# Optimization experiments

Hardware: AMD Instinct MI355X
Metric: run time of the kernel (lower is better)

The kernel has to match this reference:

```python
import jax, jax.numpy as jnp
import numpy as np

N_NODES = 100000
N_EDGES = 1600000
C_IN, C_HID, C_OUT = 32, 32, 8
N_AGENTS = 1000


def _glorot(key, shape):
    fan_in, fan_out = shape[0], shape[1]
    lim = float(np.sqrt(6.0 / (fan_in + fan_out)))
    return jax.random.uniform(key, shape, jnp.float32, -lim, lim)


def setup_inputs() -> dict:
    key = jax.random.key(0)
    ks = jax.random.split(key, 16)
    x = jax.random.normal(ks[0], (N_NODES, C_IN), jnp.float32)
    edge_index = jax.random.randint(ks[1], (2, N_EDGES), 0, N_NODES, jnp.int64)
    d = {"x": x, "edge_index": edge_index}
    dims = [(C_IN, C_HID), (C_HID, C_HID), (C_HID, C_HID)]
    for i, (di, do) in enumerate(dims, start=1):
        d[f"W_l{i}"] = _glorot(ks[2 * i], (di, do))        # neighbor (aggregated) weight
        d[f"b_l{i}"] = jnp.zeros((do,), jnp.float32)
        d[f"W_r{i}"] = _glorot(ks[2 * i + 1], (di, do))    # root/self weight (no bias)
    d["W_out"] = _glorot(ks[10], (C_HID, C_OUT))
    d["b_out"] = jnp.zeros((C_OUT,), jnp.float32)
    return d


def _sage_conv(x, src, dst, W_l, b_l, W_r):
    # mean-aggregate neighbor features at destination nodes
    msg = x[src]                                               # [E, d] gather
    summed = jax.ops.segment_sum(msg, dst, num_segments=N_NODES)
    cnt = jax.ops.segment_sum(jnp.ones((src.shape[0],), x.dtype), dst,
                              num_segments=N_NODES)
    agg = summed / jnp.maximum(cnt, 1.0)[:, None]              # deg==0 -> 0
    return agg @ W_l + b_l + x @ W_r


def reference(x, edge_index, W_l1, b_l1, W_r1, W_l2, b_l2, W_r2,
              W_l3, b_l3, W_r3, W_out, b_out):
    src, dst = edge_index[0], edge_index[1]
    h = jax.nn.relu(_sage_conv(x, src, dst, W_l1, b_l1, W_r1))
    h = jax.nn.relu(_sage_conv(h, src, dst, W_l2, b_l2, W_r2))
    h = jax.nn.relu(_sage_conv(h, src, dst, W_l3, b_l3, W_r3))
    out = h @ W_out + b_out
    return out[:N_AGENTS]
```

## Files before the change

### kernel.cpp

```cpp
#include <hip/hip_runtime.h>
#include <hip/hip_bf16.h>

#define N_NODES 100000
#define N_EDGES 1600000
#define N_AGENTS 1000

#define NB 782
#define ABLK 512
#define CHUNK (N_EDGES / ABLK)
#define CONV_BLOCKS 3125
#define FLAGS_I4 25024
#define FLAG_BLOCKS 98
#define AGRID 280

typedef short s16x8 __attribute__((ext_vector_type(8)));
typedef float f32x4 __attribute__((ext_vector_type(4)));

__device__ __forceinline__ unsigned short f2bf(float f) {
    unsigned u = __float_as_uint(f);
    u += 0x7fffu + ((u >> 16) & 1u);
    return (unsigned short)(u >> 16);
}
__device__ __forceinline__ float bflo(unsigned u) { return __uint_as_float(u << 16); }
__device__ __forceinline__ float bfhi(unsigned u) { return __uint_as_float(u & 0xffff0000u); }

__global__ __launch_bounds__(256) void hist_prep_kernel(
    const int* __restrict__ dst, int* __restrict__ partialT,
    const float* __restrict__ x, unsigned short* __restrict__ xb,
    const float* __restrict__ Wl1, const float* __restrict__ Wr1,
    const float* __restrict__ Wl2, const float* __restrict__ Wr2,
    const float* __restrict__ Wl3, const float* __restrict__ Wr3,
    unsigned short* __restrict__ Wcat, int* __restrict__ flags)
{
    int b = blockIdx.x;
    if (b < ABLK) {
        __shared__ int hist[NB];
        for (int i = threadIdx.x; i < NB; i += 256) hist[i] = 0;
        __syncthreads();
        int beg = b * CHUNK;
        for (int e = beg + threadIdx.x; e < beg + CHUNK; e += 256)
            atomicAdd(&hist[dst[e] >> 7], 1);
        __syncthreads();
        for (int i = threadIdx.x; i < NB; i += 256) partialT[i * ABLK + b] = hist[i];
    } else if (b < ABLK + CONV_BLOCKS) {
        int i = (b - ABLK) * 256 + threadIdx.x;
        float4 v = ((const float4*)x)[i];
        ((ushort4*)xb)[i] = make_ushort4(f2bf(v.x), f2bf(v.y), f2bf(v.z), f2bf(v.w));
    } else if (b < ABLK + CONV_BLOCKS + 24) {
        int gid = (b - ABLK - CONV_BLOCKS) * 256 + threadIdx.x;
        int L = gid >> 11, idx = gid & 2047;
        int k = idx >> 5, n = idx & 31;
        const float* Wl = (L == 0) ? Wl1 : (L == 1) ? Wl2 : Wl3;
        const float* Wr = (L == 0) ? Wr1 : (L == 1) ? Wr2 : Wr3;
        float v = (k < 32) ? Wl[k * 32 + n] : Wr[(k - 32) * 32 + n];
        Wcat[gid] = f2bf(v);
    } else {
        int gid = (b - ABLK - CONV_BLOCKS - 24) * 256 + threadIdx.x;
        if (gid < FLAGS_I4) ((int4*)flags)[gid] = make_int4(0, 0, 0, 0);
    }
}

__global__ __launch_bounds__(256) void bucket_prefix_kernel(
    const int* __restrict__ partialT, int* __restrict__ baseT, int* __restrict__ tot)
{
    int wave = threadIdx.x >> 6, lane = threadIdx.x & 63;
    int t = blockIdx.x * 4 + wave;
    if (t >= NB) return;
    const int4* p = (const int4*)(partialT + (size_t)t * ABLK);
    int4 u0 = p[lane * 2], u1 = p[lane * 2 + 1];
    int v0 = u0.x, v1 = u0.y, v2 = u0.z, v3 = u0.w;
    int v4 = u1.x, v5 = u1.y, v6 = u1.z, v7 = u1.w;
    int p0 = 0, p1 = v0, p2 = p1 + v1, p3 = p2 + v2;
    int p4 = p3 + v3, p5 = p4 + v4, p6 = p5 + v5, p7 = p6 + v6;
    int s = p7 + v7;
    int x = s;
    #pragma unroll
    for (int off = 1; off < 64; off <<= 1) {
        int y = __shfl_up(x, off);
        if (lane >= off) x += y;
    }
    int excl = x - s;
    int4* q = (int4*)(baseT + (size_t)t * ABLK);
    q[lane * 2]     = make_int4(excl + p0, excl + p1, excl + p2, excl + p3);
    q[lane * 2 + 1] = make_int4(excl + p4, excl + p5, excl + p6, excl + p7);
    if (lane == 63) tot[t] = x;
}

__global__ __launch_bounds__(1024) void total_scan_kernel(
    const int* __restrict__ tot, int* __restrict__ bstart)
{
    __shared__ int tmp[1024];
    int t = threadIdx.x;
    int v = (t < NB) ? tot[t] : 0;
    tmp[t] = v;
    __syncthreads();
    for (int off = 1; off < 1024; off <<= 1) {
        int u = (t >= off) ? tmp[t - off] : 0;
        __syncthreads();
        tmp[t] += u;
        __syncthreads();
    }
    if (t < NB) {
        bstart[t] = tmp[t] - v;
        if (t == NB - 1) bstart[NB] = tmp[t];
    }
}

__global__ __launch_bounds__(256) void bucket_scatter_kernel(
    const int* __restrict__ src, const int* __restrict__ dst,
    const int* __restrict__ baseT, const int* __restrict__ bstart,
    int* __restrict__ ebuf)
{
    __shared__ int cur[NB];
    int b = blockIdx.x;
    for (int i = threadIdx.x; i < NB; i += 256)
        cur[i] = bstart[i] + baseT[(size_t)i * ABLK + b];
    __syncthreads();
    int beg = b * CHUNK;
    for (int e = beg + threadIdx.x; e < beg + CHUNK; e += 256) {
        int d = dst[e];
        int slot = atomicAdd(&cur[d >> 7], 1);
        ebuf[slot] = src[e] | ((d & 127) << 17);
    }
}

__global__ __launch_bounds__(256) void bucket_csr_kernel(
    const int* __restrict__ bstart, const int* __restrict__ ebuf,
    int* __restrict__ rowptr, float* __restrict__ inv, int* __restrict__ esrc)
{
    __shared__ int hist4[512], cur4[512], tmp[256];
    int b = blockIdx.x;
    int t = threadIdx.x;
    int beg = bstart[b], end = bstart[b + 1];
    hist4[t] = 0; hist4[t + 256] = 0;
    __syncthreads();
    for (int i = beg + t; i < end; i += 256) {
        int p = ebuf[i];
        int ln = (p >> 17) & 127;
        int cls = (p & 0x1FFFF) >> 15;
        atomicAdd(&hist4[ln * 4 + cls], 1);
    }
    __syncthreads();
    int c0 = 0, c1 = 0, c2 = 0, c3 = 0, v = 0;
    if (t < 128) {
        c0 = hist4[t * 4 + 0]; c1 = hist4[t * 4 + 1];
        c2 = hist4[t * 4 + 2]; c3 = hist4[t * 4 + 3];
        v = c0 + c1 + c2 + c3;
    }
    tmp[t] = v;
    __syncthreads();
    for (int off = 1; off < 256; off <<= 1) {
        int u = (t >= off) ? tmp[t - off] : 0;
        __syncthreads();
        tmp[t] += u;
        __syncthreads();
    }
    int excl = tmp[t] - v;
    int node = b * 128 + t;
    if (t < 128 && node < N_NODES) {
        int start = beg + excl;
        rowptr[node] = start;
        inv[node] = 1.0f / fmaxf((float)v, 1.0f);
        cur4[t * 4 + 0] = start;
        cur4[t * 4 + 1] = start + c0;
        cur4[t * 4 + 2] = start + c0 + c1;
        cur4[t * 4 + 3] = start + c0 + c1 + c2;
    }
    if (b == NB - 1 && t == 0) rowptr[N_NODES] = N_EDGES;
    __syncthreads();
    for (int i = beg + t; i < end; i += 256) {
        int p = ebuf[i];
        int ln = (p >> 17) & 127;
        int s = p & 0x1FFFF;
        int slot = atomicAdd(&cur4[ln * 4 + (s >> 15)], 1);
        esrc[slot] = s;
    }
}

__global__ __launch_bounds__(256) void active_mark_kernel(
    const int* __restrict__ rowptr, const int* __restrict__ esrc,
    int* __restrict__ flags, int* __restrict__ acount)
{
    int gid = blockIdx.x * 256 + threadIdx.x;
    if (gid == 0) *acount = 0;
    if (gid < N_AGENTS) flags[gid] = 1;
    int e1 = rowptr[N_AGENTS];
    for (int j = gid; j < e1; j += gridDim.x * 256)
        flags[esrc[j]] = 1;
}

__global__ __launch_bounds__(256) void active_compact_kernel(
    const int* __restrict__ flags, int* __restrict__ alist, int* __restrict__ acount)
{
    int gid = blockIdx.x * 256 + threadIdx.x;
    int f = (gid < N_NODES) ? flags[gid] : 0;
    int lane = threadIdx.x & 63, wave = threadIdx.x >> 6;
    unsigned long long m = __ballot(f != 0);
    int pre = __popcll(m & ((1ull << lane) - 1ull));
    __shared__ int wbase[4];
    __shared__ int bbase;
    if (lane == 0) wbase[wave] = __popcll(m);
    __syncthreads();
    if (threadIdx.x == 0) {
        int t0 = wbase[0], t1 = t0 + wbase[1], t2 = t1 + wbase[2];
        int tot = t2 + wbase[3];
        bbase = atomicAdd(acount, tot);
        wbase[0] = 0; wbase[1] = t0; wbase[2] = t1; wbase[3] = t2;
    }
    __syncthreads();
    if (f) alist[bbase + wbase[wave] + pre] = gid;
}

__global__ __launch_bounds__(256) void sage_fused_kernel(
    const int* __restrict__ rowptr, const int* __restrict__ esrc,
    const float* __restrict__ inv, const unsigned short* __restrict__ hb,
    const unsigned short* __restrict__ Wcat, const float* __restrict__ bl,
    const float* __restrict__ Wout, const float* __restrict__ bout,
    void* __restrict__ outp, int n_nodes, int final)
{
    __shared__ unsigned short sW[2048];
    __shared__ float sb[32];
    __shared__ unsigned short smean[64 * 40];
    __shared__ float sh3[64 * 33];
    __shared__ float sWo[256];
    __shared__ float sbo[8];

    int tid = threadIdx.x;
    ((uint4*)sW)[tid] = ((const uint4*)Wcat)[tid];
    if (tid < 32) sb[tid] = bl[tid];
    if (final) {
        sWo[tid] = Wout[tid];
        if (tid < 8) sbo[tid] = bout[tid];
    }

    int lane = tid & 63, wave = tid >> 6;

    int g = lane >> 2, q = lane & 3;
    int nodeA = blockIdx.x * 64 + wave * 16 + g;
    int beg = 0, end = 0;
    if (nodeA < n_nodes) { beg = rowptr[nodeA]; end = rowptr[nodeA + 1]; }
    float a0 = 0.f, a1 = 0.f, a2 = 0.f, a3 = 0.f;
    float a4 = 0.f, a5 = 0.f, a6 = 0.f, a7 = 0.f;
    int j = beg;
    for (; j + 3 < end; j += 4) {
        int s0 = esrc[j];
        int s1 = esrc[j + 1];
        int s2 = esrc[j + 2];
        int s3 = esrc[j + 3];
        uint4 u0 = *(const uint4*)(hb + s0 * 32 + q * 8);
        uint4 u1 = *(const uint4*)(hb + s1 * 32 + q * 8);
        uint4 u2 = *(const uint4*)(hb + s2 * 32 + q * 8);
        uint4 u3 = *(const uint4*)(hb + s3 * 32 + q * 8);
        a0 += bflo(u0.x); a1 += bfhi(u0.x);
        a2 += bflo(u0.y); a3 += bfhi(u0.y);
        a4 += bflo(u0.z); a5 += bfhi(u0.z);
        a6 += bflo(u0.w); a7 += bfhi(u0.w);
        a0 += bflo(u1.x); a1 += bfhi(u1.x);
        a2 += bflo(u1.y); a3 += bfhi(u1.y);
        a4 += bflo(u1.z); a5 += bfhi(u1.z);
        a6 += bflo(u1.w); a7 += bfhi(u1.w);
        a0 += bflo(u2.x); a1 += bfhi(u2.x);
        a2 += bflo(u2.y); a3 += bfhi(u2.y);
        a4 += bflo(u2.z); a5 += bfhi(u2.z);
        a6 += bflo(u2.w); a7 += bfhi(u2.w);
        a0 += bflo(u3.x); a1 += bfhi(u3.x);
        a2 += bflo(u3.y); a3 += bfhi(u3.y);
        a4 += bflo(u3.z); a5 += bfhi(u3.z);
        a6 += bflo(u3.w); a7 += bfhi(u3.w);
    }
    for (; j < end; j++) {
        int s = esrc[j];
        uint4 u = *(const uint4*)(hb + s * 32 + q * 8);
        a0 += bflo(u.x); a1 += bfhi(u.x);
        a2 += bflo(u.y); a3 += bfhi(u.y);
        a4 += bflo(u.z); a5 += bfhi(u.z);
        a6 += bflo(u.w); a7 += bfhi(u.w);
    }
    float iv = (nodeA < n_nodes) ? inv[nodeA] : 0.f;
    uint4 o;
    o.x = (unsigned)f2bf(a0 * iv) | ((unsigned)f2bf(a1 * iv) << 16);
    o.y = (unsigned)f2bf(a2 * iv) | ((unsigned)f2bf(a3 * iv) << 16);
    o.z = (unsigned)f2bf(a4 * iv) | ((unsigned)f2bf(a5 * iv) << 16);
    o.w = (unsigned)f2bf(a6 * iv) | ((unsigned)f2bf(a7 * iv) << 16);
    int mrow = wave * 16 + g;
    *(uint4*)&smean[mrow * 40 + q * 8] = o;
    __syncthreads();

    int l15 = lane & 15, quad = lane >> 4;
    s16x8 bf_[2][2];
    #pragma unroll
    for (int kt = 0; kt < 2; kt++)
        #pragma unroll
        for (int nt = 0; nt < 2; nt++)
            #pragma unroll
            for (int jj = 0; jj < 8; jj++) {
                int k = kt * 32 + quad * 8 + jj;
                bf_[kt][nt][jj] = (short)sW[k * 32 + l15 + nt * 16];
            }
    float bias0 = sb[l15], bias1 = sb[l15 + 16];

    int tilebase = blockIdx.x * 64 + wave * 16;
    int nodeD = tilebase + l15;
    int na = min(nodeD, n_nodes - 1);
    s16x8 am = *(const s16x8*)&smean[(wave * 16 + l15) * 40 + quad * 8];
    s16x8 as = *(const s16x8*)(hb + (size_t)na * 32 + quad * 8);
    f32x4 acc0 = {0.f, 0.f, 0.f, 0.f};
    f32x4 acc1 = {0.f, 0.f, 0.f, 0.f};
    acc0 = __builtin_amdgcn_mfma_f32_16x16x32_bf16(am, bf_[0][0], acc0, 0, 0, 0);
    acc0 = __builtin_amdgcn_mfma_f32_16x16x32_bf16(as, bf_[1][0], acc0, 0, 0, 0);
    acc1 = __builtin_amdgcn_mfma_f32_16x16x32_bf16(am, bf_[0][1], acc1, 0, 0, 0);
    acc1 = __builtin_amdgcn_mfma_f32_16x16x32_bf16(as, bf_[1][1], acc1, 0, 0, 0);

    if (!final) {
        #pragma unroll
        for (int r = 0; r < 4; r++) {
            int onode = tilebase + quad * 4 + r;
            if (onode < n_nodes) {
                ((unsigned short*)outp)[onode * 32 + l15]      = f2bf(fmaxf(acc0[r] + bias0, 0.f));
                ((unsigned short*)outp)[onode * 32 + l15 + 16] = f2bf(fmaxf(acc1[r] + bias1, 0.f));
            }
        }
    } else {
        #pragma unroll
        for (int r = 0; r < 4; r++) {
            int row = wave * 16 + quad * 4 + r;
            sh3[row * 33 + l15]      = fmaxf(acc0[r] + bias0, 0.f);
            sh3[row * 33 + l15 + 16] = fmaxf(acc1[r] + bias1, 0.f);
        }
        __syncthreads();
        #pragma unroll
        for (int i = tid; i < 512; i += 256) {
            int ln = i >> 3, c = i & 7;
            int gn = blockIdx.x * 64 + ln;
            if (gn < N_AGENTS) {
                float ov = sbo[c];
                #pragma unroll
                for (int k = 0; k < 32; k++) ov += sh3[ln * 33 + k] * sWo[k * 8 + c];
                ((float*)outp)[gn * 8 + c] = ov;
            }
        }
    }
}

__global__ __launch_bounds__(256) void sage_fused_act_kernel(
    const int* __restrict__ rowptr, const int* __restrict__ esrc,
    const float* __restrict__ inv, const unsigned short* __restrict__ hb,
    const unsigned short* __restrict__ Wcat, const float* __restrict__ bl,
    unsigned short* __restrict__ outp,
    const int* __restrict__ alist, const int* __restrict__ acount)
{
    __shared__ unsigned short sW[2048];
    __shared__ float sb[32];
    __shared__ unsigned short smean[64 * 40];
    __shared__ int sids[64];

    int tid = threadIdx.x;
    int count = *acount;
    ((uint4*)sW)[tid] = ((const uint4*)Wcat)[tid];
    if (tid < 32) sb[tid] = bl[tid];
    __syncthreads();

    int lane = tid & 63, wave = tid >> 6;
    int g = lane >> 2, q = lane & 3;
    int l15 = lane & 15, quad = lane >> 4;

    s16x8 bf_[2][2];
    #pragma unroll
    for (int kt = 0; kt < 2; kt++)
        #pragma unroll
        for (int nt = 0; nt < 2; nt++)
            #pragma unroll
            for (int jj = 0; jj < 8; jj++) {
                int k = kt * 32 + quad * 8 + jj;
                bf_[kt][nt][jj] = (short)sW[k * 32 + l15 + nt * 16];
            }
    float bias0 = sb[l15], bias1 = sb[l15 + 16];

    for (int tile = blockIdx.x; tile * 64 < count; tile += gridDim.x) {
        if (tid < 64)
            sids[tid] = (tile * 64 + tid < count) ? alist[tile * 64 + tid] : -1;
        __syncthreads();

        int nodeA = sids[wave * 16 + g];
        int beg = 0, end = 0;
        if (nodeA >= 0) { beg = rowptr[nodeA]; end = rowptr[nodeA + 1]; }
        float a0 = 0.f, a1 = 0.f, a2 = 0.f, a3 = 0.f;
        float a4 = 0.f, a5 = 0.f, a6 = 0.f, a7 = 0.f;
        int j = beg;
        for (; j + 3 < end; j += 4) {
            int s0 = esrc[j];
            int s1 = esrc[j + 1];
            int s2 = esrc[j + 2];
            int s3 = esrc[j + 3];
            uint4 u0 = *(const uint4*)(hb + s0 * 32 + q * 8);
            uint4 u1 = *(const uint4*)(hb + s1 * 32 + q * 8);
            uint4 u2 = *(const uint4*)(hb + s2 * 32 + q * 8);
            uint4 u3 = *(const uint4*)(hb + s3 * 32 + q * 8);
            a0 += bflo(u0.x); a1 += bfhi(u0.x);
            a2 += bflo(u0.y); a3 += bfhi(u0.y);
            a4 += bflo(u0.z); a5 += bfhi(u0.z);
            a6 += bflo(u0.w); a7 += bfhi(u0.w);
            a0 += bflo(u1.x); a1 += bfhi(u1.x);
            a2 += bflo(u1.y); a3 += bfhi(u1.y);
            a4 += bflo(u1.z); a5 += bfhi(u1.z);
            a6 += bflo(u1.w); a7 += bfhi(u1.w);
            a0 += bflo(u2.x); a1 += bfhi(u2.x);
            a2 += bflo(u2.y); a3 += bfhi(u2.y);
            a4 += bflo(u2.z); a5 += bfhi(u2.z);
            a6 += bflo(u2.w); a7 += bfhi(u2.w);
            a0 += bflo(u3.x); a1 += bfhi(u3.x);
            a2 += bflo(u3.y); a3 += bfhi(u3.y);
            a4 += bflo(u3.z); a5 += bfhi(u3.z);
            a6 += bflo(u3.w); a7 += bfhi(u3.w);
        }
        for (; j < end; j++) {
            int s = esrc[j];
            uint4 u = *(const uint4*)(hb + s * 32 + q * 8);
            a0 += bflo(u.x); a1 += bfhi(u.x);
            a2 += bflo(u.y); a3 += bfhi(u.y);
            a4 += bflo(u.z); a5 += bfhi(u.z);
            a6 += bflo(u.w); a7 += bfhi(u.w);
        }
        float iv = (nodeA >= 0) ? inv[nodeA] : 0.f;
        uint4 o;
        o.x = (unsigned)f2bf(a0 * iv) | ((unsigned)f2bf(a1 * iv) << 16);
        o.y = (unsigned)f2bf(a2 * iv) | ((unsigned)f2bf(a3 * iv) << 16);
        o.z = (unsigned)f2bf(a4 * iv) | ((unsigned)f2bf(a5 * iv) << 16);
        o.w = (unsigned)f2bf(a6 * iv) | ((unsigned)f2bf(a7 * iv) << 16);
        int mrow = wave * 16 + g;
        *(uint4*)&smean[mrow * 40 + q * 8] = o;
        __syncthreads();

        int nd = sids[wave * 16 + l15];
        int na = (nd >= 0) ? nd : 0;
        s16x8 am = *(const s16x8*)&smean[(wave * 16 + l15) * 40 + quad * 8];
        s16x8 as = *(const s16x8*)(hb + (size_t)na * 32 + quad * 8);
        f32x4 acc0 = {0.f, 0.f, 0.f, 0.f};
        f32x4 acc1 = {0.f, 0.f, 0.f, 0.f};
        acc0 = __builtin_amdgcn_mfma_f32_16x16x32_bf16(am, bf_[0][0], acc0, 0, 0, 0);
        acc0 = __builtin_amdgcn_mfma_f32_16x16x32_bf16(as, bf_[1][0], acc0, 0, 0, 0);
        acc1 = __builtin_amdgcn_mfma_f32_16x16x32_bf16(am, bf_[0][1], acc1, 0, 0, 0);
        acc1 = __builtin_amdgcn_mfma_f32_16x16x32_bf16(as, bf_[1][1], acc1, 0, 0, 0);

        #pragma unroll
        for (int r = 0; r < 4; r++) {
            int onode = sids[wave * 16 + quad * 4 + r];
            if (onode >= 0) {
                outp[onode * 32 + l15]      = f2bf(fmaxf(acc0[r] + bias0, 0.f));
                outp[onode * 32 + l15 + 16] = f2bf(fmaxf(acc1[r] + bias1, 0.f));
            }
        }
        __syncthreads();
    }
}

extern "C" void kernel_launch(void* const* d_in, const int* in_sizes, int n_in,
                              void* d_out, int out_size, void* d_ws, size_t ws_size,
                              hipStream_t stream) {
    const float* x   = (const float*)d_in[0];
    const int* ei    = (const int*)d_in[1];
    const float* Wl1 = (const float*)d_in[2];
    const float* bl1 = (const float*)d_in[3];
    const float* Wr1 = (const float*)d_in[4];
    const float* Wl2 = (const float*)d_in[5];
    const float* bl2 = (const float*)d_in[6];
    const float* Wr2 = (const float*)d_in[7];
    const float* Wl3 = (const float*)d_in[8];
    const float* bl3 = (const float*)d_in[9];
    const float* Wr3 = (const float*)d_in[10];
    const float* Wout = (const float*)d_in[11];
    const float* bout = (const float*)d_in[12];
    float* out = (float*)d_out;

    const int* src = ei;
    const int* dst = ei + N_EDGES;

    char* ws = (char*)d_ws;
    int*   rowptr   = (int*)ws;                                ws += (size_t)(N_NODES + 8) * 4;
    float* inv      = (float*)ws;                              ws += (size_t)N_NODES * 4;
    int*   partialT = (int*)ws;                                ws += (size_t)NB * ABLK * 4;
    int*   baseT    = (int*)ws;                                ws += (size_t)NB * ABLK * 4;
    int*   tot      = (int*)ws;                                ws += 784 * 4;
    int*   bstart   = (int*)ws;                                ws += 784 * 4;
    int*   esrc     = (int*)ws;                                ws += (size_t)N_EDGES * 4;
    unsigned short* hXb   = (unsigned short*)ws;               ws += (size_t)N_NODES * 32 * 2;
    unsigned short* hAb   = (unsigned short*)ws;               ws += (size_t)N_NODES * 32 * 2;
    unsigned short* hBb   = (unsigned short*)ws;               ws += (size_t)N_NODES * 32 * 2;
    unsigned short* Wcat  = (unsigned short*)ws;               ws += 3 * 2048 * 2;
    int*   flags    = (int*)ws;                                ws += (size_t)100096 * 4;
    int*   alist    = (int*)ws;                                ws += (size_t)100096 * 4;
    int*   acount   = (int*)ws;                                ws += 16;
    int*   ebuf     = (int*)hAb;

    hist_prep_kernel<<<ABLK + CONV_BLOCKS + 24 + FLAG_BLOCKS, 256, 0, stream>>>(
        dst, partialT, x, hXb, Wl1, Wr1, Wl2, Wr2, Wl3, Wr3, Wcat, flags);
    bucket_prefix_kernel<<<(NB + 3) / 4, 256, 0, stream>>>(partialT, baseT, tot);
    total_scan_kernel<<<1, 1024, 0, stream>>>(tot, bstart);
    bucket_scatter_kernel<<<ABLK, 256, 0, stream>>>(src, dst, baseT, bstart, ebuf);
    bucket_csr_kernel<<<NB, 256, 0, stream>>>(bstart, ebuf, rowptr, inv, esrc);

    active_mark_kernel<<<64, 256, 0, stream>>>(rowptr, esrc, flags, acount);
    active_compact_kernel<<<(N_NODES + 255) / 256, 256, 0, stream>>>(flags, alist, acount);

    sage_fused_kernel<<<(N_NODES + 63) / 64, 256, 0, stream>>>(
        rowptr, esrc, inv, hXb, Wcat, bl1, Wout, bout, hAb, N_NODES, 0);
    sage_fused_act_kernel<<<AGRID, 256, 0, stream>>>(
        rowptr, esrc, inv, hAb, Wcat + 2048, bl2, hBb, alist, acount);
    sage_fused_kernel<<<(N_AGENTS + 63) / 64, 256, 0, stream>>>(
        rowptr, esrc, inv, hBb, Wcat + 4096, bl3, Wout, bout, out, N_AGENTS, 1);
}
```

Before: 195.2 us.

## Fold total scan into scatter and active-node marking into CSR build

Removes the single-block total_scan kernel by having every bucket_scatter block redundantly scan the bucket totals, with block 0 writing bstart. Active-node flag marking moves into bucket_csr_kernel, and the compaction kernel is dropped. Layer 2 then runs over all node tiles and skips unflagged nodes, instead of looping over a compacted list. This cuts three kernel launches and their serialization, but spends redundant scan work in each scatter block and launches many mostly-idle blocks in layer 2.

Measured after the change: 185.1 us. 1.05x faster.

```diff
diff --git a/kernel.cpp b/kernel.cpp
--- a/kernel.cpp
+++ b/kernel.cpp
@@ -11,7 +11,6 @@
 #define CONV_BLOCKS 3125
 #define FLAGS_I4 25024
 #define FLAG_BLOCKS 98
-#define AGRID 280
 
 typedef short s16x8 __attribute__((ext_vector_type(8)));
 typedef float f32x4 __attribute__((ext_vector_type(4)));
@@ -86,35 +85,41 @@
     if (lane == 63) tot[t] = x;
 }
 
-__global__ __launch_bounds__(1024) void total_scan_kernel(
-    const int* __restrict__ tot, int* __restrict__ bstart)
-{
-    __shared__ int tmp[1024];
-    int t = threadIdx.x;
-    int v = (t < NB) ? tot[t] : 0;
-    tmp[t] = v;
-    __syncthreads();
-    for (int off = 1; off < 1024; off <<= 1) {
-        int u = (t >= off) ? tmp[t - off] : 0;
-        __syncthreads();
-        tmp[t] += u;
-        __syncthreads();
-    }
-    if (t < NB) {
-        bstart[t] = tmp[t] - v;
-        if (t == NB - 1) bstart[NB] = tmp[t];
-    }
-}
-
 __global__ __launch_bounds__(256) void bucket_scatter_kernel(
     const int* __restrict__ src, const int* __restrict__ dst,
-    const int* __restrict__ baseT, const int* __restrict__ bstart,
-    int* __restrict__ ebuf)
+    const int* __restrict__ baseT, const int* __restrict__ tot,
+    int* __restrict__ bstart, int* __restrict__ ebuf)
 {
     __shared__ int cur[NB];
-    int b = blockIdx.x;
-    for (int i = threadIdx.x; i < NB; i += 256)
-        cur[i] = bstart[i] + baseT[(size_t)i * ABLK + b];
+    __shared__ int tsum[256];
+    int b = blockIdx.x, t = threadIdx.x;
+    int i0 = t * 4;
+    int v0 = (i0     < NB) ? tot[i0]     : 0;
+    int v1 = (i0 + 1 < NB) ? tot[i0 + 1] : 0;
+    int v2 = (i0 + 2 < NB) ? tot[i0 + 2] : 0;
+    int v3 = (i0 + 3 < NB) ? tot[i0 + 3] : 0;
+    int p1 = v0, p2 = v0 + v1, p3 = v0 + v1 + v2, s4 = p3 + v3;
+    tsum[t] = s4;
+    __syncthreads();
+    for (int off = 1; off < 256; off <<= 1) {
+        int u = (t >= off) ? tsum[t - off] : 0;
+        __syncthreads();
+        tsum[t] += u;
+        __syncthreads();
+    }
+    int excl = tsum[t] - s4;
+    int st0 = excl, st1 = excl + p1, st2 = excl + p2, st3 = excl + p3;
+    if (i0     < NB) cur[i0]     = st0 + baseT[(size_t)i0 * ABLK + b];
+    if (i0 + 1 < NB) cur[i0 + 1] = st1 + baseT[(size_t)(i0 + 1) * ABLK + b];
+    if (i0 + 2 < NB) cur[i0 + 2] = st2 + baseT[(size_t)(i0 + 2) * ABLK + b];
+    if (i0 + 3 < NB) cur[i0 + 3] = st3 + baseT[(size_t)(i0 + 3) * ABLK + b];
+    if (b == 0) {
+        if (i0     < NB) bstart[i0]     = st0;
+        if (i0 + 1 < NB) bstart[i0 + 1] = st1;
+        if (i0 + 2 < NB) bstart[i0 + 2] = st2;
+        if (i0 + 3 < NB) bstart[i0 + 3] = st3;
+        if (t == 255)    bstart[NB] = tsum[255];
+    }
     __syncthreads();
     int beg = b * CHUNK;
     for (int e = beg + threadIdx.x; e < beg + CHUNK; e += 256) {
@@ -126,7 +131,8 @@
 
 __global__ __launch_bounds__(256) void bucket_csr_kernel(
     const int* __restrict__ bstart, const int* __restrict__ ebuf,
-    int* __restrict__ rowptr, float* __restrict__ inv, int* __restrict__ esrc)
+    int* __restrict__ rowptr, float* __restrict__ inv, int* __restrict__ esrc,
+    int* __restrict__ flags)
 {
     __shared__ int hist4[512], cur4[512], tmp[256];
     int b = blockIdx.x;
@@ -165,50 +171,20 @@
         cur4[t * 4 + 1] = start + c0;
         cur4[t * 4 + 2] = start + c0 + c1;
         cur4[t * 4 + 3] = start + c0 + c1 + c2;
+        if (node < N_AGENTS) flags[node] = 1;
     }
     if (b == NB - 1 && t == 0) rowptr[N_NODES] = N_EDGES;
     __syncthreads();
+    bool agent_bucket = (b < 8);
     for (int i = beg + t; i < end; i += 256) {
         int p = ebuf[i];
         int ln = (p >> 17) & 127;
         int s = p & 0x1FFFF;
         int slot = atomicAdd(&cur4[ln * 4 + (s >> 15)], 1);
         esrc[slot] = s;
-    }
-}
-
-__global__ __launch_bounds__(256) void active_mark_kernel(
-    const int* __restrict__ rowptr, const int* __restrict__ esrc,
-    int* __restrict__ flags, int* __restrict__ acount)
-{
-    int gid = blockIdx.x * 256 + threadIdx.x;
-    if (gid == 0) *acount = 0;
-    if (gid < N_AGENTS) flags[gid] = 1;
-    int e1 = rowptr[N_AGENTS];
-    for (int j = gid; j < e1; j += gridDim.x * 256)
-        flags[esrc[j]] = 1;
-}
-
-__global__ __launch_bounds__(256) void active_compact_kernel(
-    const int* __restrict__ flags, int* __restrict__ alist, int* __restrict__ acount)
-{
-    int gid = blockIdx.x * 256 + threadIdx.x;
-    int f = (gid < N_NODES) ? flags[gid] : 0;
-    int lane = threadIdx.x & 63, wave = threadIdx.x >> 6;
-    unsigned long long m = __ballot(f != 0);
-    int pre = __popcll(m & ((1ull << lane) - 1ull));
-    __shared__ int wbase[4];
-    __shared__ int bbase;
-    if (lane == 0) wbase[wave] = __popcll(m);
-    __syncthreads();
-    if (threadIdx.x == 0) {
-        int t0 = wbase[0], t1 = t0 + wbase[1], t2 = t1 + wbase[2];
-        int tot = t2 + wbase[3];
-        bbase = atomicAdd(acount, tot);
-        wbase[0] = 0; wbase[1] = t0; wbase[2] = t1; wbase[3] = t2;
-    }
-    __syncthreads();
-    if (f) alist[bbase + wbase[wave] + pre] = gid;
+        if (agent_bucket && (b * 128 + ln) < N_AGENTS)
+            flags[s] = 1;
+    }
 }
 
 __global__ __launch_bounds__(256) void sage_fused_kernel(
@@ -342,28 +318,81 @@
     }
 }
 
-__global__ __launch_bounds__(256) void sage_fused_act_kernel(
+__global__ __launch_bounds__(256) void sage_fused_flag_kernel(
     const int* __restrict__ rowptr, const int* __restrict__ esrc,
     const float* __restrict__ inv, const unsigned short* __restrict__ hb,
     const unsigned short* __restrict__ Wcat, const float* __restrict__ bl,
-    unsigned short* __restrict__ outp,
-    const int* __restrict__ alist, const int* __restrict__ acount)
+    unsigned short* __restrict__ outp, const int* __restrict__ flags,
+    int n_nodes)
 {
     __shared__ unsigned short sW[2048];
     __shared__ float sb[32];
     __shared__ unsigned short smean[64 * 40];
-    __shared__ int sids[64];
+    __shared__ int sflag[64];
 
     int tid = threadIdx.x;
-    int count = *acount;
     ((uint4*)sW)[tid] = ((const uint4*)Wcat)[tid];
     if (tid < 32) sb[tid] = bl[tid];
+    if (tid < 64) {
+        int gid = blockIdx.x * 64 + tid;
+        sflag[tid] = (gid < n_nodes) ? flags[gid] : 0;
+    }
     __syncthreads();
 
     int lane = tid & 63, wave = tid >> 6;
+
     int g = lane >> 2, q = lane & 3;
+    int lnode = wave * 16 + g;
+    int nodeA = blockIdx.x * 64 + lnode;
+    int beg = 0, end = 0;
+    if (sflag[lnode]) { beg = rowptr[nodeA]; end = rowptr[nodeA + 1]; }
+    float a0 = 0.f, a1 = 0.f, a2 = 0.f, a3 = 0.f;
+    float a4 = 0.f, a5 = 0.f, a6 = 0.f, a7 = 0.f;
+    int j = beg;
+    for (; j + 3 < end; j += 4) {
+        int s0 = esrc[j];
+        int s1 = esrc[j + 1];
+        int s2 = esrc[j + 2];
+        int s3 = esrc[j + 3];
+        uint4 u0 = *(const uint4*)(hb + s0 * 32 + q * 8);
+        uint4 u1 = *(const uint4*)(hb + s1 * 32 + q * 8);
+        uint4 u2 = *(const uint4*)(hb + s2 * 32 + q * 8);
+        uint4 u3 = *(const uint4*)(hb + s3 * 32 + q * 8);
+        a0 += bflo(u0.x); a1 += bfhi(u0.x);
+        a2 += bflo(u0.y); a3 += bfhi(u0.y);
+        a4 += bflo(u0.z); a5 += bfhi(u0.z);
+        a6 += bflo(u0.w); a7 += bfhi(u0.w);
+        a0 += bflo(u1.x); a1 += bfhi(u1.x);
+        a2 += bflo(u1.y); a3 += bfhi(u1.y);
+        a4 += bflo(u1.z); a5 += bfhi(u1.z);
+        a6 += bflo(u1.w); a7 += bfhi(u1.w);
+        a0 += bflo(u2.x); a1 += bfhi(u2.x);
+        a2 += bflo(u2.y); a3 += bfhi(u2.y);
+        a4 += bflo(u2.z); a5 += bfhi(u2.z);
+        a6 += bflo(u2.w); a7 += bfhi(u2.w);
+        a0 += bflo(u3.x); a1 += bfhi(u3.x);
+        a2 += bflo(u3.y); a3 += bfhi(u3.y);
+        a4 += bflo(u3.z); a5 += bfhi(u3.z);
+        a6 += bflo(u3.w); a7 += bfhi(u3.w);
+    }
+    for (; j < end; j++) {
+        int s = esrc[j];
+        uint4 u = *(const uint4*)(hb + s * 32 + q * 8);
+        a0 += bflo(u.x); a1 += bfhi(u.x);
+        a2 += bflo(u.y); a3 += bfhi(u.y);
+        a4 += bflo(u.z); a5 += bfhi(u.z);
+        a6 += bflo(u.w); a7 += bfhi(u.w);
+    }
+    float iv = sflag[lnode] ? inv[nodeA] : 0.f;
+    uint4 o;
+    o.x = (unsigned)f2bf(a0 * iv) | ((unsigned)f2bf(a1 * iv) << 16);
+    o.y = (unsigned)f2bf(a2 * iv) | ((unsigned)f2bf(a3 * iv) << 16);
+    o.z = (unsigned)f2bf(a4 * iv) | ((unsigned)f2bf(a5 * iv) << 16);
+    o.w = (unsigned)f2bf(a6 * iv) | ((unsigned)f2bf(a7 * iv) << 16);
+    *(uint4*)&smean[lnode * 40 + q * 8] = o;
+    __syncthreads();
+
     int l15 = lane & 15, quad = lane >> 4;
-
     s16x8 bf_[2][2];
     #pragma unroll
     for (int kt = 0; kt < 2; kt++)
@@ -376,81 +405,26 @@
             }
     float bias0 = sb[l15], bias1 = sb[l15 + 16];
 
-    for (int tile = blockIdx.x; tile * 64 < count; tile += gridDim.x) {
-        if (tid < 64)
-            sids[tid] = (tile * 64 + tid < count) ? alist[tile * 64 + tid] : -1;
-        __syncthreads();
-
-        int nodeA = sids[wave * 16 + g];
-        int beg = 0, end = 0;
-        if (nodeA >= 0) { beg = rowptr[nodeA]; end = rowptr[nodeA + 1]; }
-        float a0 = 0.f, a1 = 0.f, a2 = 0.f, a3 = 0.f;
-        float a4 = 0.f, a5 = 0.f, a6 = 0.f, a7 = 0.f;
-        int j = beg;
-        for (; j + 3 < end; j += 4) {
-            int s0 = esrc[j];
-            int s1 = esrc[j + 1];
-            int s2 = esrc[j + 2];
-            int s3 = esrc[j + 3];
-            uint4 u0 = *(const uint4*)(hb + s0 * 32 + q * 8);
-            uint4 u1 = *(const uint4*)(hb + s1 * 32 + q * 8);
-            uint4 u2 = *(const uint4*)(hb + s2 * 32 + q * 8);
-            uint4 u3 = *(const uint4*)(hb + s3 * 32 + q * 8);
-            a0 += bflo(u0.x); a1 += bfhi(u0.x);
-            a2 += bflo(u0.y); a3 += bfhi(u0.y);
-            a4 += bflo(u0.z); a5 += bfhi(u0.z);
-            a6 += bflo(u0.w); a7 += bfhi(u0.w);
-            a0 += bflo(u1.x); a1 += bfhi(u1.x);
-            a2 += bflo(u1.y); a3 += bfhi(u1.y);
-            a4 += bflo(u1.z); a5 += bfhi(u1.z);
-            a6 += bflo(u1.w); a7 += bfhi(u1.w);
-            a0 += bflo(u2.x); a1 += bfhi(u2.x);
-            a2 += bflo(u2.y); a3 += bfhi(u2.y);
-            a4 += bflo(u2.z); a5 += bfhi(u2.z);
-            a6 += bflo(u2.w); a7 += bfhi(u2.w);
-            a0 += bflo(u3.x); a1 += bfhi(u3.x);
-            a2 += bflo(u3.y); a3 += bfhi(u3.y);
-            a4 += bflo(u3.z); a5 += bfhi(u3.z);
-            a6 += bflo(u3.w); a7 += bfhi(u3.w);
+    int tilebase = blockIdx.x * 64 + wave * 16;
+    int nodeD = tilebase + l15;
+    int na = min(nodeD, n_nodes - 1);
+    s16x8 am = *(const s16x8*)&smean[(wave * 16 + l15) * 40 + quad * 8];
+    s16x8 as = *(const s16x8*)(hb + (size_t)na * 32 + quad * 8);
+    f32x4 acc0 = {0.f, 0.f, 0.f, 0.f};
+    f32x4 acc1 = {0.f, 0.f, 0.f, 0.f};
+    acc0 = __builtin_amdgcn_mfma_f32_16x16x32_bf16(am, bf_[0][0], acc0, 0, 0, 0);
+    acc0 = __builtin_amdgcn_mfma_f32_16x16x32_bf16(as, bf_[1][0], acc0, 0, 0, 0);
+    acc1 = __builtin_amdgcn_mfma_f32_16x16x32_bf16(am, bf_[0][1], acc1, 0, 0, 0);
+    acc1 = __builtin_amdgcn_mfma_f32_16x16x32_bf16(as, bf_[1][1], acc1, 0, 0, 0);
+
+    #pragma unroll
+    for (int r = 0; r < 4; r++) {
+        int lr = wave * 16 + quad * 4 + r;
+        int onode = tilebase + quad * 4 + r;
+        if (onode < n_nodes && sflag[lr]) {
+            outp[onode * 32 + l15]      = f2bf(fmaxf(acc0[r] + bias0, 0.f));
+            outp[onode * 32 + l15 + 16] = f2bf(fmaxf(acc1[r] + bias1, 0.f));
         }
-        for (; j < end; j++) {
-            int s = esrc[j];
-            uint4 u = *(const uint4*)(hb + s * 32 + q * 8);
-            a0 += bflo(u.x); a1 += bfhi(u.x);
-            a2 += bflo(u.y); a3 += bfhi(u.y);
-            a4 += bflo(u.z); a5 += bfhi(u.z);
-            a6 += bflo(u.w); a7 += bfhi(u.w);
-        }
-        float iv = (nodeA >= 0) ? inv[nodeA] : 0.f;
-        uint4 o;
-        o.x = (unsigned)f2bf(a0 * iv) | ((unsigned)f2bf(a1 * iv) << 16);
-        o.y = (unsigned)f2bf(a2 * iv) | ((unsigned)f2bf(a3 * iv) << 16);
-        o.z = (unsigned)f2bf(a4 * iv) | ((unsigned)f2bf(a5 * iv) << 16);
-        o.w = (unsigned)f2bf(a6 * iv) | ((unsigned)f2bf(a7 * iv) << 16);
-        int mrow = wave * 16 + g;
-        *(uint4*)&smean[mrow * 40 + q * 8] = o;
-        __syncthreads();
-
-        int nd = sids[wave * 16 + l15];
-        int na = (nd >= 0) ? nd : 0;
-        s16x8 am = *(const s16x8*)&smean[(wave * 16 + l15) * 40 + quad * 8];
-        s16x8 as = *(const s16x8*)(hb + (size_t)na * 32 + quad * 8);
-        f32x4 acc0 = {0.f, 0.f, 0.f, 0.f};
-        f32x4 acc1 = {0.f, 0.f, 0.f, 0.f};
-        acc0 = __builtin_amdgcn_mfma_f32_16x16x32_bf16(am, bf_[0][0], acc0, 0, 0, 0);
-        acc0 = __builtin_amdgcn_mfma_f32_16x16x32_bf16(as, bf_[1][0], acc0, 0, 0, 0);
-        acc1 = __builtin_amdgcn_mfma_f32_16x16x32_bf16(am, bf_[0][1], acc1, 0, 0, 0);
-        acc1 = __builtin_amdgcn_mfma_f32_16x16x32_bf16(as, bf_[1][1], acc1, 0, 0, 0);
-
-        #pragma unroll
-        for (int r = 0; r < 4; r++) {
-            int onode = sids[wave * 16 + quad * 4 + r];
-            if (onode >= 0) {
-                outp[onode * 32 + l15]      = f2bf(fmaxf(acc0[r] + bias0, 0.f));
-                outp[onode * 32 + l15 + 16] = f2bf(fmaxf(acc1[r] + bias1, 0.f));
-            }
-        }
-        __syncthreads();
     }
 }
 
@@ -488,24 +462,18 @@
     unsigned short* hBb   = (unsigned short*)ws;               ws += (size_t)N_NODES * 32 * 2;
     unsigned short* Wcat  = (unsigned short*)ws;               ws += 3 * 2048 * 2;
     int*   flags    = (int*)ws;                                ws += (size_t)100096 * 4;
-    int*   alist    = (int*)ws;                                ws += (size_t)100096 * 4;
-    int*   acount   = (int*)ws;                                ws += 16;
     int*   ebuf     = (int*)hAb;
 
     hist_prep_kernel<<<ABLK + CONV_BLOCKS + 24 + FLAG_BLOCKS, 256, 0, stream>>>(
         dst, partialT, x, hXb, Wl1, Wr1, Wl2, Wr2, Wl3, Wr3, Wcat, flags);
     bucket_prefix_kernel<<<(NB + 3) / 4, 256, 0, stream>>>(partialT, baseT, tot);
-    total_scan_kernel<<<1, 1024, 0, stream>>>(tot, bstart);
-    bucket_scatter_kernel<<<ABLK, 256, 0, stream>>>(src, dst, baseT, bstart, ebuf);
-    bucket_csr_kernel<<<NB, 256, 0, stream>>>(bstart, ebuf, rowptr, inv, esrc);
-
-    active_mark_kernel<<<64, 256, 0, stream>>>(rowptr, esrc, flags, acount);
-    active_compact_kernel<<<(N_NODES + 255) / 256, 256, 0, stream>>>(flags, alist, acount);
+    bucket_scatter_kernel<<<ABLK, 256, 0, stream>>>(src, dst, baseT, tot, bstart, ebuf);
+    bucket_csr_kernel<<<NB, 256, 0, stream>>>(bstart, ebuf, rowptr, inv, esrc, flags);
 
     sage_fused_kernel<<<(N_NODES + 63) / 64, 256, 0, stream>>>(
         rowptr, esrc, inv, hXb, Wcat, bl1, Wout, bout, hAb, N_NODES, 0);
-    sage_fused_act_kernel<<<AGRID, 256, 0, stream>>>(
-        rowptr, esrc, inv, hAb, Wcat + 2048, bl2, hBb, alist, acount);
+    sage_fused_flag_kernel<<<(N_NODES + 63) / 64, 256, 0, stream>>>(
+        rowptr, esrc, inv, hAb, Wcat + 2048, bl2, hBb, flags, N_NODES);
     sage_fused_kernel<<<(N_AGENTS + 63) / 64, 256, 0, stream>>>(
         rowptr, esrc, inv, hBb, Wcat + 4096, bl3, Wout, bout, out, N_AGENTS, 1);
 }
```
